# Optimization experiments

Hardware: AMD Instinct MI355X
Metric: run time of the kernel (lower is better)

Reference implementation:

```python
import jax, jax.numpy as jnp
import numpy as np

B, C, H, W = 2, 256, 64, 64
NUM_HEADS = 4
HEAD_DIM = C // NUM_HEADS
N = H * W


def setup_inputs() -> dict:
    key = jax.random.key(0)
    ks = jax.random.split(key, 10)
    x = jax.random.normal(ks[0], (B, C, H, W), dtype=jnp.float32)
    # mostly-True mask; diagonal forced True so every row has a valid key
    m = jax.random.uniform(ks[1], (B, N, N)) > 0.1
    spatial_mask = m | jnp.eye(N, dtype=bool)[None]
    s = 1.0 / np.sqrt(C)
    wq = jax.random.normal(ks[2], (C, C), dtype=jnp.float32) * s
    bq = jnp.zeros((C,), jnp.float32)
    wk = jax.random.normal(ks[3], (C, C), dtype=jnp.float32) * s
    bk = jnp.zeros((C,), jnp.float32)
    wv = jax.random.normal(ks[4], (C, C), dtype=jnp.float32) * s
    bv = jnp.zeros((C,), jnp.float32)
    # torch zero-inits out_proj; use random weights for a non-trivial baseline
    wo = jax.random.normal(ks[5], (C, C), dtype=jnp.float32) * s
    bo = jnp.zeros((C,), jnp.float32)
    return {"x": x, "spatial_mask": spatial_mask, "wq": wq, "bq": bq,
            "wk": wk, "bk": bk, "wv": wv, "bv": bv, "wo": wo, "bo": bo}


def reference(x, spatial_mask, wq, bq, wk, bk, wv, bv, wo, bo):
    b, c, h, w = x.shape
    n = h * w
    nh, hd = NUM_HEADS, HEAD_DIM
    scale = hd ** -0.5
    x_flat = x.reshape(b, c, n).transpose(0, 2, 1)           # [b, n, c]
    q = (x_flat @ wq.T + bq).reshape(b, n, nh, hd).transpose(0, 2, 1, 3)
    k = (x_flat @ wk.T + bk).reshape(b, n, nh, hd).transpose(0, 2, 1, 3)
    v = (x_flat @ wv.T + bv).reshape(b, n, nh, hd).transpose(0, 2, 1, 3)
    logits = jnp.einsum('bhqd,bhkd->bhqk', q, k) * scale      # [b, nh, n, n]
    logits = jnp.where(spatial_mask[:, None], logits, -jnp.inf)
    attn = jax.nn.softmax(logits, axis=-1)                    # dropout = identity (eval)
    out = jnp.einsum('bhqk,bhkd->bhqd', attn, v)              # [b, nh, n, hd]
    out = out.transpose(0, 2, 1, 3).reshape(b, n, c)
    out = out @ wo.T + bo
    return out.transpose(0, 2, 1).reshape(b, c, h, w)
```

## Files before the change

### kernel.cpp

```cpp
#include <hip/hip_runtime.h>
#include <math.h>

namespace {
constexpr int B_    = 2;
constexpr int C_    = 256;
constexpr int NHEAD = 4;
constexpr int HDIM  = 64;
constexpr int NTOK  = 4096;
constexpr float SCALE = 0.125f;
constexpr float LOG2E = 1.44269504f;
}

typedef _Float16 half8  __attribute__((ext_vector_type(8)));
typedef _Float16 half4  __attribute__((ext_vector_type(4)));
typedef __fp16   fp16x2 __attribute__((ext_vector_type(2)));
typedef float    floatx4 __attribute__((ext_vector_type(4)));
typedef int      int4v   __attribute__((ext_vector_type(4)));
typedef unsigned int uint2v __attribute__((ext_vector_type(2)));

__device__ __forceinline__ void plswap32(int &a, int &b) {
#if __has_builtin(__builtin_amdgcn_permlane32_swap)
    const uint2v r = __builtin_amdgcn_permlane32_swap((unsigned)a, (unsigned)b, false, false);
    a = (int)r[0]; b = (int)r[1];
#else
    asm volatile("s_nop 1\n\tv_permlane32_swap_b32 %0, %1\n\ts_nop 1"
                 : "+v"(a), "+v"(b));
#endif
}
__device__ __forceinline__ void plswap16(int &a, int &b) {
#if __has_builtin(__builtin_amdgcn_permlane16_swap)
    const uint2v r = __builtin_amdgcn_permlane16_swap((unsigned)a, (unsigned)b, false, false);
    a = (int)r[0]; b = (int)r[1];
#else
    asm volatile("s_nop 1\n\tv_permlane16_swap_b32 %0, %1\n\ts_nop 1"
                 : "+v"(a), "+v"(b));
#endif
}

__device__ __forceinline__ void gload_lds16(const _Float16* g, _Float16* l, int lane) {
#if __has_builtin(__builtin_amdgcn_global_load_lds)
    __builtin_amdgcn_global_load_lds(
        (const __attribute__((address_space(1))) void*)g,
        (__attribute__((address_space(3))) void*)l, 16, 0, 0);
#else
    *(half8*)((char*)l + lane * 16) = *(const half8*)g;
#endif
}

__global__ __launch_bounds__(256) void pack_mask(
    const unsigned int* __restrict__ m32, unsigned int* __restrict__ packed)
{
    int c0 = 0, c1 = 0, c2 = 0, c3 = 0;
    #pragma unroll
    for (int i = 0; i < 16; i++) {
        const unsigned int d = m32[i];
        c0 += (d == 0x00000001u);
        c1 += (d == 0x3F803F80u);
        c2 += (d == 0x3F800000u);
        c3 += (d == 0x01010101u);
    }
    int fmt = 1, best = c1;
    if (c0 > best) { best = c0; fmt = 0; }
    if (c2 > best) { best = c2; fmt = 2; }
    if (c3 > best) { best = c3; fmt = 3; }

    const unsigned int W = blockIdx.x * 256 + threadIdx.x;
    unsigned int bits = 0;
    if (fmt == 1) {
        const uint4* p4 = (const uint4*)(m32 + (size_t)W * 16);
        #pragma unroll
        for (int i = 0; i < 4; i++) {
            const uint4 v = p4[i];
            const unsigned int d[4] = { v.x, v.y, v.z, v.w };
            #pragma unroll
            for (int j = 0; j < 4; j++) {
                const int e = i * 8 + j * 2;
                bits |= ((d[j] & 0xFFFFu) ? 1u : 0u) << e;
                bits |= ((d[j] >> 16)     ? 1u : 0u) << (e + 1);
            }
        }
    } else if (fmt != 3) {
        const uint4* p4 = (const uint4*)(m32 + (size_t)W * 32);
        #pragma unroll
        for (int i = 0; i < 8; i++) {
            const uint4 v = p4[i];
            bits |= (v.x ? 1u : 0u) << (i * 4 + 0);
            bits |= (v.y ? 1u : 0u) << (i * 4 + 1);
            bits |= (v.z ? 1u : 0u) << (i * 4 + 2);
            bits |= (v.w ? 1u : 0u) << (i * 4 + 3);
        }
    } else {
        const uint4* p4 = (const uint4*)(m32 + (size_t)W * 8);
        #pragma unroll
        for (int i = 0; i < 2; i++) {
            const uint4 v = p4[i];
            const unsigned int d[4] = { v.x, v.y, v.z, v.w };
            #pragma unroll
            for (int j = 0; j < 4; j++) {
                const int e = (i * 4 + j) * 4;
                bits |= ((d[j] & 0x000000FFu) ? 1u : 0u) << (e + 0);
                bits |= ((d[j] & 0x0000FF00u) ? 1u : 0u) << (e + 1);
                bits |= ((d[j] & 0x00FF0000u) ? 1u : 0u) << (e + 2);
                bits |= ((d[j] & 0xFF000000u) ? 1u : 0u) << (e + 3);
            }
        }
    }
    packed[W] = bits;
}

__global__ __launch_bounds__(256) void qkv_mfma(
    const float* __restrict__ x,
    const float* __restrict__ wq, const float* __restrict__ bq,
    const float* __restrict__ wk, const float* __restrict__ bk,
    const float* __restrict__ wv, const float* __restrict__ bv,
    _Float16* __restrict__ qo, _Float16* __restrict__ ko,
    _Float16* __restrict__ vo)
{
    const int nt = blockIdx.x;
    const int b  = blockIdx.y;
    const int p  = blockIdx.z;

    const float* w; const float* bias;
    if (p == 0)      { w = wq; bias = bq; }
    else if (p == 1) { w = wk; bias = bk; }
    else             { w = wv; bias = bv; }

    const int t    = threadIdx.x;
    const int wid  = t >> 6;
    const int lane = t & 63;
    const int quad = lane >> 4;
    const int l15  = lane & 15;
    const int n0   = nt * 64;

    __shared__ _Float16 xsh[64 * 264];
    __shared__ _Float16 wsh[64 * 72];
    __shared__ _Float16 tbuf[64 * 72];

    const int srow = t >> 2;
    const int sc   = (t & 3) * 16;

    {
        const int cr = t >> 4;
        const int nu = (t & 15) * 4;
        const float* xb = x + (size_t)b * C_ * NTOK;
        #pragma unroll
        for (int cc = 0; cc < 16; cc++) {
            const int cl = cc * 16 + cr;
            const float4 v = *(const float4*)&xb[(size_t)cl * NTOK + n0 + nu];
            xsh[(nu + 0) * 264 + cl] = (_Float16)v.x;
            xsh[(nu + 1) * 264 + cl] = (_Float16)v.y;
            xsh[(nu + 2) * 264 + cl] = (_Float16)v.z;
            xsh[(nu + 3) * 264 + cl] = (_Float16)v.w;
        }
    }

    for (int h = 0; h < NHEAD; h++) {
        const int co0 = h * 64;
        floatx4 acc[4];
        #pragma unroll
        for (int i = 0; i < 4; i++) acc[i] = (floatx4)0.f;

        for (int c0 = 0; c0 < C_; c0 += 64) {
            {
                const float* wr = &w[(size_t)(co0 + srow) * C_ + c0 + sc];
                half8 h0, h1;
                #pragma unroll
                for (int u = 0; u < 2; u++) {
                    const float4 a = *(const float4*)&wr[u * 4];
                    h0[u*4+0]=(_Float16)a.x; h0[u*4+1]=(_Float16)a.y;
                    h0[u*4+2]=(_Float16)a.z; h0[u*4+3]=(_Float16)a.w;
                }
                #pragma unroll
                for (int u = 0; u < 2; u++) {
                    const float4 a = *(const float4*)&wr[8 + u * 4];
                    h1[u*4+0]=(_Float16)a.x; h1[u*4+1]=(_Float16)a.y;
                    h1[u*4+2]=(_Float16)a.z; h1[u*4+3]=(_Float16)a.w;
                }
                *(half8*)&wsh[srow * 72 + sc]     = h0;
                *(half8*)&wsh[srow * 72 + sc + 8] = h1;
            }
            __syncthreads();
            const half8 a0 = *(const half8*)&wsh[(wid * 16 + l15) * 72 + quad * 8];
            const half8 a1 = *(const half8*)&wsh[(wid * 16 + l15) * 72 + 32 + quad * 8];
            #pragma unroll
            for (int nt2 = 0; nt2 < 4; nt2++) {
                const half8 b0 = *(const half8*)&xsh[(nt2 * 16 + l15) * 264 + c0 + quad * 8];
                const half8 b1 = *(const half8*)&xsh[(nt2 * 16 + l15) * 264 + c0 + 32 + quad * 8];
                acc[nt2] = __builtin_amdgcn_mfma_f32_16x16x32_f16(a0, b0, acc[nt2], 0, 0, 0);
                acc[nt2] = __builtin_amdgcn_mfma_f32_16x16x32_f16(a1, b1, acc[nt2], 0, 0, 0);
            }
            __syncthreads();
        }

        const float4 bb4 = *(const float4*)&bias[co0 + wid * 16 + quad * 4];
        const float bb[4] = { bb4.x, bb4.y, bb4.z, bb4.w };

        if (p < 2) {
            const float osc = (p == 0) ? (SCALE * LOG2E) : 1.0f;
            #pragma unroll
            for (int nt2 = 0; nt2 < 4; nt2++) {
                half4 hv;
                #pragma unroll
                for (int i = 0; i < 4; i++)
                    hv[i] = (_Float16)((acc[nt2][i] + bb[i]) * osc);
                *(half4*)&tbuf[(nt2 * 16 + l15) * 72 + wid * 16 + quad * 4] = hv;
            }
            __syncthreads();
            _Float16* dh = (p == 0 ? qo : ko) + (size_t)(b * NHEAD + h) * NTOK * HDIM;
            const half8 o0 = *(const half8*)&tbuf[srow * 72 + sc];
            const half8 o1 = *(const half8*)&tbuf[srow * 72 + sc + 8];
            *(half8*)&dh[(size_t)(n0 + srow) * HDIM + sc]     = o0;
            *(half8*)&dh[(size_t)(n0 + srow) * HDIM + sc + 8] = o1;
        } else {
            #pragma unroll
            for (int nt2 = 0; nt2 < 4; nt2++)
                #pragma unroll
                for (int i = 0; i < 4; i++)
                    tbuf[(wid * 16 + quad * 4 + i) * 72 + nt2 * 16 + l15] =
                        (_Float16)(acc[nt2][i] + bb[i]);
            __syncthreads();
            _Float16* vth = vo + (size_t)(b * NHEAD + h) * HDIM * NTOK;
            const half8 o0 = *(const half8*)&tbuf[srow * 72 + sc];
            const half8 o1 = *(const half8*)&tbuf[srow * 72 + sc + 8];
            *(half8*)&vth[(size_t)srow * NTOK + n0 + sc]     = o0;
            *(half8*)&vth[(size_t)srow * NTOK + n0 + sc + 8] = o1;
        }
        __syncthreads();
    }
}

__global__ __launch_bounds__(512) void attn(
    const _Float16* __restrict__ q, const _Float16* __restrict__ k,
    const _Float16* __restrict__ vt, const unsigned int* __restrict__ mpacked,
    _Float16* __restrict__ ao)
{
    const int b  = blockIdx.z;
    const int h  = blockIdx.y;
    const int q0 = blockIdx.x * 64;
    const int t    = threadIdx.x;
    const int w    = t >> 6;
    const int lane = t & 63;
    const int quad = lane >> 4;
    const int l15  = lane & 15;
    const int half = w >> 2;
    const int w4   = w & 3;
    const int koff = half * (NTOK / 2);

    __shared__ __align__(16) char smem_raw[65536];
    _Float16* const sbase = (_Float16*)(smem_raw + half * 32768);

    const size_t head_off = (size_t)(b * NHEAD + h) * NTOK * HDIM;
    const _Float16* qb  = q  + head_off;
    const _Float16* kb  = k  + head_off;
    const _Float16* vtb = vt + head_off;
    const unsigned int* mrow = mpacked + (size_t)b * NTOK * 128;

    const int qrow = q0 + w4 * 16 + l15;
    half8 aq0 = *(const half8*)&qb[(size_t)qrow * HDIM + quad * 8];
    half8 aq1 = *(const half8*)&qb[(size_t)qrow * HDIM + 32 + quad * 8];
    const unsigned int* mq = &mrow[(size_t)qrow * 128];

    const int jr  = l15 & 7;
    const int xs0 = (quad ^ jr) << 3;
    const int xs1 = ((quad + 4) ^ jr) << 3;

    uint2 mw = *(const uint2*)&mq[koff >> 5];
    uint2 mw_nxt = mw;

    float l_loc = 0.f;
    floatx4 o_acc[4];
    #pragma unroll
    for (int i = 0; i < 4; i++) o_acc[i] = (floatx4)0.f;

#define STAGE(WO, K0N)                                                        \
    {                                                                         \
        const int rl = lane >> 3;                       \
        const int xc = ((lane & 7) ^ rl) << 3;        \
        const int c0 = w4 * 2, c1 = c0 + 1;                                   \
        gload_lds16(&kb[(size_t)((K0N) + c0 * 8 + rl) * HDIM + xc],           \
                    &sbase[(WO) + c0 * 512], lane);                           \
        gload_lds16(&kb[(size_t)((K0N) + c1 * 8 + rl) * HDIM + xc],           \
                    &sbase[(WO) + c1 * 512], lane);                           \
        gload_lds16(&vtb[(size_t)(c0 * 8 + rl) * NTOK + (K0N) + xc],          \
                    &sbase[(WO) + 4096 + c0 * 512], lane);                    \
        gload_lds16(&vtb[(size_t)(c1 * 8 + rl) * NTOK + (K0N) + xc],          \
                    &sbase[(WO) + 4096 + c1 * 512], lane);                    \
    }

    STAGE(0, koff)
    __syncthreads();

#define SOFTMAX_CT(CT, WORD, SH, Pa, Pb)                                          \
    {                                                                             \
        const unsigned nib = ((WORD) >> ((SH) + quad * 4)) & 0xFu;                \
        const float p0 = __builtin_amdgcn_exp2f((nib & 1u) ? sa[CT][0] : -3.0e38f);\
        const float p1 = __builtin_amdgcn_exp2f((nib & 2u) ? sa[CT][1] : -3.0e38f);\
        const float p2 = __builtin_amdgcn_exp2f((nib & 4u) ? sa[CT][2] : -3.0e38f);\
        const float p3 = __builtin_amdgcn_exp2f((nib & 8u) ? sa[CT][3] : -3.0e38f);\
        l_loc += (p0 + p1) + (p2 + p3);                                           \
        Pa = __builtin_bit_cast(int, __builtin_amdgcn_cvt_pkrtz(p0, p1));         \
        Pb = __builtin_bit_cast(int, __builtin_amdgcn_cvt_pkrtz(p2, p3));         \
    }

#define ATTN_TILE(RO, WO, KT, PF)                                                 \
    {                                                                             \
        if (PF) {                                                                 \
            const int k0n = koff + (KT) * 64 + 64;                                \
            STAGE(WO, k0n)                                                        \
            mw_nxt = *(const uint2*)&mq[k0n >> 5];                                \
        }                                                                         \
        floatx4 sa[4];                                                            \
        __builtin_amdgcn_s_setprio(1);                                            \
        _Pragma("unroll")                                                         \
        for (int ct = 0; ct < 4; ct++) {                                          \
            sa[ct] = (floatx4)0.f;                                                \
            const half8 ka0 = *(const half8*)&sbase[(RO) + (ct*16 + l15)*64 + xs0];\
            const half8 ka1 = *(const half8*)&sbase[(RO) + (ct*16 + l15)*64 + xs1];\
            sa[ct] = __builtin_amdgcn_mfma_f32_16x16x32_f16(ka0, aq0, sa[ct], 0, 0, 0);     \
            sa[ct] = __builtin_amdgcn_mfma_f32_16x16x32_f16(ka1, aq1, sa[ct], 0, 0, 0);     \
        }                                                                         \
        __builtin_amdgcn_s_setprio(0);                                            \
        int P00, P01, P10, P11, P20, P21, P30, P31;                               \
        SOFTMAX_CT(0, mw.x, 0,  P00, P01)                                         \
        SOFTMAX_CT(1, mw.x, 16, P10, P11)                                         \
        SOFTMAX_CT(2, mw.y, 0,  P20, P21)                                         \
        SOFTMAX_CT(3, mw.y, 16, P30, P31)                                         \
        mw = mw_nxt;                                                              \
                                                   \
        plswap32(P00, P10); plswap32(P01, P11);                                   \
        plswap32(P20, P30); plswap32(P21, P31);                                   \
                                               \
        plswap16(P00, P10); plswap16(P01, P11);                                   \
        plswap16(P20, P30); plswap16(P21, P31);                                   \
        const half8 pb0 = __builtin_bit_cast(half8, (int4v){P00, P01, P10, P11}); \
        const half8 pb1 = __builtin_bit_cast(half8, (int4v){P20, P21, P30, P31}); \
        __builtin_amdgcn_s_setprio(1);                                            \
        _Pragma("unroll")                                                         \
        for (int dt = 0; dt < 4; dt++) {                                          \
            const half8 va0 = *(const half8*)&sbase[(RO) + 4096 + (dt*16 + l15)*64 + xs0];\
            const half8 va1 = *(const half8*)&sbase[(RO) + 4096 + (dt*16 + l15)*64 + xs1];\
            o_acc[dt] = __builtin_amdgcn_mfma_f32_16x16x32_f16(va0, pb0, o_acc[dt], 0, 0, 0);      \
            o_acc[dt] = __builtin_amdgcn_mfma_f32_16x16x32_f16(va1, pb1, o_acc[dt], 0, 0, 0);      \
        }                                                                         \
        __builtin_amdgcn_s_setprio(0);                                            \
        __syncthreads();                                                          \
    }

    for (int kt2 = 0; kt2 < 15; kt2++) {
        ATTN_TILE(0,    8192, 2 * kt2,     1)
        ATTN_TILE(8192, 0,    2 * kt2 + 1, 1)
    }
    ATTN_TILE(0,    8192, 30, 1)
    ATTN_TILE(8192, 0,    31, 0)

#undef ATTN_TILE
#undef SOFTMAX_CT
#undef STAGE

    l_loc += __shfl_xor(l_loc, 16, 64);
    l_loc += __shfl_xor(l_loc, 32, 64);

    float* oex = (float*)smem_raw;
    float* lex = (float*)(smem_raw + 16384);
    if (w >= 4) {
        float* dst = &oex[((size_t)(w - 4) * 64 + lane) * 16];
        #pragma unroll
        for (int dt = 0; dt < 4; dt++)
            *(floatx4*)&dst[dt * 4] = o_acc[dt];
        if (quad == 0) lex[(w - 4) * 16 + l15] = l_loc;
    }
    __syncthreads();
    if (w < 4) {
        const float* src = &oex[((size_t)w * 64 + lane) * 16];
        const float lt = l_loc + lex[w * 16 + l15];
        const float inv = (lt > 0.f) ? (1.0f / lt) : 0.f;
        _Float16* aob = ao + ((size_t)b * NTOK + q0 + w * 16 + l15) * C_ + h * 64;
        #pragma unroll
        for (int dt = 0; dt < 4; dt++) {
            const floatx4 o2 = *(const floatx4*)&src[dt * 4];
            half4 r;
            #pragma unroll
            for (int rr = 0; rr < 4; rr++)
                r[rr] = (_Float16)((o_acc[dt][rr] + o2[rr]) * inv);
            *(half4*)&aob[dt * 16 + quad * 4] = r;
        }
    }
}

__global__ __launch_bounds__(256) void out_mfma(
    const _Float16* __restrict__ ao, const float* __restrict__ wo,
    const float* __restrict__ bo, float* __restrict__ out)
{
    const int nt  = blockIdx.x;
    const int cot = blockIdx.y;
    const int b   = blockIdx.z;
    const int t    = threadIdx.x;
    const int wid  = t >> 6;
    const int lane = t & 63;
    const int quad = lane >> 4;
    const int l15  = lane & 15;
    const int n0  = nt * 64;
    const int co0 = cot * 64;

    __shared__ _Float16 wsh[64 * 72];
    __shared__ _Float16 ash[64 * 72];
    __shared__ float    tf[64 * 68];

    const int srow = t >> 2;
    const int sc   = (t & 3) * 16;

    floatx4 acc[4];
    #pragma unroll
    for (int i = 0; i < 4; i++) acc[i] = (floatx4)0.f;

    const _Float16* aob = ao + ((size_t)b * NTOK + n0) * C_;

    for (int c0 = 0; c0 < C_; c0 += 64) {
        {
            const float* wr = &wo[(size_t)(co0 + srow) * C_ + c0 + sc];
            half8 h0, h1;
            #pragma unroll
            for (int u = 0; u < 2; u++) {
                const float4 a = *(const float4*)&wr[u * 4];
                h0[u*4+0]=(_Float16)a.x; h0[u*4+1]=(_Float16)a.y;
                h0[u*4+2]=(_Float16)a.z; h0[u*4+3]=(_Float16)a.w;
            }
            #pragma unroll
            for (int u = 0; u < 2; u++) {
                const float4 a = *(const float4*)&wr[8 + u * 4];
                h1[u*4+0]=(_Float16)a.x; h1[u*4+1]=(_Float16)a.y;
                h1[u*4+2]=(_Float16)a.z; h1[u*4+3]=(_Float16)a.w;
            }
            *(half8*)&wsh[srow * 72 + sc]     = h0;
            *(half8*)&wsh[srow * 72 + sc + 8] = h1;
        }
        {
            const _Float16* ar = &aob[(size_t)srow * C_ + c0 + sc];
            *(half8*)&ash[srow * 72 + sc]     = *(const half8*)&ar[0];
            *(half8*)&ash[srow * 72 + sc + 8] = *(const half8*)&ar[8];
        }
        __syncthreads();
        const half8 a0 = *(const half8*)&wsh[(wid * 16 + l15) * 72 + quad * 8];
        const half8 a1 = *(const half8*)&wsh[(wid * 16 + l15) * 72 + 32 + quad * 8];
        #pragma unroll
        for (int nt2 = 0; nt2 < 4; nt2++) {
            const half8 b0 = *(const half8*)&ash[(nt2 * 16 + l15) * 72 + quad * 8];
            const half8 b1 = *(const half8*)&ash[(nt2 * 16 + l15) * 72 + 32 + quad * 8];
            acc[nt2] = __builtin_amdgcn_mfma_f32_16x16x32_f16(a0, b0, acc[nt2], 0, 0, 0);
            acc[nt2] = __builtin_amdgcn_mfma_f32_16x16x32_f16(a1, b1, acc[nt2], 0, 0, 0);
        }
        __syncthreads();
    }

    #pragma unroll
    for (int nt2 = 0; nt2 < 4; nt2++)
        #pragma unroll
        for (int i = 0; i < 4; i++)
            tf[(wid * 16 + quad * 4 + i) * 68 + nt2 * 16 + l15] = acc[nt2][i];
    __syncthreads();

    const int row = t >> 2;
    const int c4  = (t & 3) * 16;
    const float bb = bo[co0 + row];
    float* orow = &out[((size_t)(b * C_ + co0 + row)) * NTOK + n0 + c4];
    #pragma unroll
    for (int u = 0; u < 4; u++) {
        float4 v = *(const float4*)&tf[row * 68 + c4 + u * 4];
        v.x += bb; v.y += bb; v.z += bb; v.w += bb;
        *(float4*)&orow[u * 4] = v;
    }
}

extern "C" void kernel_launch(void* const* d_in, const int* in_sizes, int n_in,
                              void* d_out, int out_size, void* d_ws, size_t ws_size,
                              hipStream_t stream) {
    const float* x    = (const float*)d_in[0];
    const void*  mask = d_in[1];
    const float* wq   = (const float*)d_in[2];
    const float* bq   = (const float*)d_in[3];
    const float* wk   = (const float*)d_in[4];
    const float* bk   = (const float*)d_in[5];
    const float* wv   = (const float*)d_in[6];
    const float* bv   = (const float*)d_in[7];
    const float* wo   = (const float*)d_in[8];
    const float* bo   = (const float*)d_in[9];
    float* out = (float*)d_out;

    const size_t qkv_elems = (size_t)B_ * NHEAD * NTOK * HDIM;
    _Float16* wsh = (_Float16*)d_ws;
    _Float16* qbuf  = wsh;
    _Float16* kbuf  = wsh + qkv_elems;
    _Float16* vtbuf = wsh + 2 * qkv_elems;
    _Float16* aobuf = wsh + 3 * qkv_elems;
    unsigned int* mpacked = (unsigned int*)(wsh + 4 * qkv_elems);

    pack_mask<<<dim3((B_ * NTOK * 128) / 256), 256, 0, stream>>>(
        (const unsigned int*)mask, mpacked);
    qkv_mfma<<<dim3(NTOK / 64, B_, 3), 256, 0, stream>>>(
        x, wq, bq, wk, bk, wv, bv, qbuf, kbuf, vtbuf);
    attn<<<dim3(NTOK / 64, NHEAD, B_), 512, 0, stream>>>(
        qbuf, kbuf, vtbuf, mpacked, aobuf);
    out_mfma<<<dim3(NTOK / 64, C_ / 64, B_), 256, 0, stream>>>(
        aobuf, wo, bo, out);
}
```

Baseline: 296.4 us.

## Pre-convert projection weights to fp16 once and read MFMA operands directly

Adds a small kernel that converts the four projection weight matrices to fp16 once per call, so the QKV and output projection kernels no longer convert fp32 weights per tile. Both projection kernels drop their LDS staging of weight tiles, and the output kernel also drops LDS staging of the attention output, loading MFMA operands straight from global memory with no per-iteration barriers. This removes redundant conversion work and synchronization, but adds a kernel launch and relies on cache for reuse of operands that LDS used to share across waves.

```diff
diff --git a/kernel.cpp b/kernel.cpp
--- a/kernel.cpp
+++ b/kernel.cpp
@@ -47,6 +47,23 @@
 #endif
 }
 
+__global__ __launch_bounds__(256) void wprep(
+    const float* __restrict__ wq, const float* __restrict__ wk,
+    const float* __restrict__ wv, const float* __restrict__ wo,
+    _Float16* __restrict__ w16)
+{
+    const float* src = (blockIdx.y == 0) ? wq :
+                       (blockIdx.y == 1) ? wk :
+                       (blockIdx.y == 2) ? wv : wo;
+    const int i8 = (blockIdx.x * 256 + threadIdx.x) * 8;
+    const float4 a = *(const float4*)&src[i8];
+    const float4 b = *(const float4*)&src[i8 + 4];
+    half8 h;
+    h[0]=(_Float16)a.x; h[1]=(_Float16)a.y; h[2]=(_Float16)a.z; h[3]=(_Float16)a.w;
+    h[4]=(_Float16)b.x; h[5]=(_Float16)b.y; h[6]=(_Float16)b.z; h[7]=(_Float16)b.w;
+    *(half8*)&w16[(size_t)blockIdx.y * 65536 + i8] = h;
+}
+
 __global__ __launch_bounds__(256) void pack_mask(
     const unsigned int* __restrict__ m32, unsigned int* __restrict__ packed)
 {
@@ -109,10 +126,9 @@
 }
 
 __global__ __launch_bounds__(256) void qkv_mfma(
-    const float* __restrict__ x,
-    const float* __restrict__ wq, const float* __restrict__ bq,
-    const float* __restrict__ wk, const float* __restrict__ bk,
-    const float* __restrict__ wv, const float* __restrict__ bv,
+    const float* __restrict__ x, const _Float16* __restrict__ w16,
+    const float* __restrict__ bq, const float* __restrict__ bk,
+    const float* __restrict__ bv,
     _Float16* __restrict__ qo, _Float16* __restrict__ ko,
     _Float16* __restrict__ vo)
 {
@@ -120,10 +136,8 @@
     const int b  = blockIdx.y;
     const int p  = blockIdx.z;
 
-    const float* w; const float* bias;
-    if (p == 0)      { w = wq; bias = bq; }
-    else if (p == 1) { w = wk; bias = bk; }
-    else             { w = wv; bias = bv; }
+    const _Float16* w = w16 + (size_t)p * C_ * C_;
+    const float* bias = (p == 0) ? bq : (p == 1) ? bk : bv;
 
     const int t    = threadIdx.x;
     const int wid  = t >> 6;
@@ -133,7 +147,6 @@
     const int n0   = nt * 64;
 
     __shared__ _Float16 xsh[64 * 264];
-    __shared__ _Float16 wsh[64 * 72];
     __shared__ _Float16 tbuf[64 * 72];
 
     const int srow = t >> 2;
@@ -153,6 +166,9 @@
             xsh[(nu + 3) * 264 + cl] = (_Float16)v.w;
         }
     }
+    __syncthreads();
+
+    const _Float16* wrow = &w[(size_t)(wid * 16 + l15) * C_];
 
     for (int h = 0; h < NHEAD; h++) {
         const int co0 = h * 64;
@@ -160,28 +176,10 @@
         #pragma unroll
         for (int i = 0; i < 4; i++) acc[i] = (floatx4)0.f;
 
+        #pragma unroll
         for (int c0 = 0; c0 < C_; c0 += 64) {
-            {
-                const float* wr = &w[(size_t)(co0 + srow) * C_ + c0 + sc];
-                half8 h0, h1;
-                #pragma unroll
-                for (int u = 0; u < 2; u++) {
-                    const float4 a = *(const float4*)&wr[u * 4];
-                    h0[u*4+0]=(_Float16)a.x; h0[u*4+1]=(_Float16)a.y;
-                    h0[u*4+2]=(_Float16)a.z; h0[u*4+3]=(_Float16)a.w;
-                }
-                #pragma unroll
-                for (int u = 0; u < 2; u++) {
-                    const float4 a = *(const float4*)&wr[8 + u * 4];
-                    h1[u*4+0]=(_Float16)a.x; h1[u*4+1]=(_Float16)a.y;
-                    h1[u*4+2]=(_Float16)a.z; h1[u*4+3]=(_Float16)a.w;
-                }
-                *(half8*)&wsh[srow * 72 + sc]     = h0;
-                *(half8*)&wsh[srow * 72 + sc + 8] = h1;
-            }
-            __syncthreads();
-            const half8 a0 = *(const half8*)&wsh[(wid * 16 + l15) * 72 + quad * 8];
-            const half8 a1 = *(const half8*)&wsh[(wid * 16 + l15) * 72 + 32 + quad * 8];
+            const half8 a0 = *(const half8*)&wrow[(size_t)co0 * C_ + c0 + quad * 8];
+            const half8 a1 = *(const half8*)&wrow[(size_t)co0 * C_ + c0 + 32 + quad * 8];
             #pragma unroll
             for (int nt2 = 0; nt2 < 4; nt2++) {
                 const half8 b0 = *(const half8*)&xsh[(nt2 * 16 + l15) * 264 + c0 + quad * 8];
@@ -189,7 +187,6 @@
                 acc[nt2] = __builtin_amdgcn_mfma_f32_16x16x32_f16(a0, b0, acc[nt2], 0, 0, 0);
                 acc[nt2] = __builtin_amdgcn_mfma_f32_16x16x32_f16(a1, b1, acc[nt2], 0, 0, 0);
             }
-            __syncthreads();
         }
 
         const float4 bb4 = *(const float4*)&bias[co0 + wid * 16 + quad * 4];
@@ -326,10 +323,8 @@
         SOFTMAX_CT(2, mw.y, 0,  P20, P21)                                         \
         SOFTMAX_CT(3, mw.y, 16, P30, P31)                                         \
         mw = mw_nxt;                                                              \
-                                                   \
         plswap32(P00, P10); plswap32(P01, P11);                                   \
         plswap32(P20, P30); plswap32(P21, P31);                                   \
-                                               \
         plswap16(P00, P10); plswap16(P01, P11);                                   \
         plswap16(P20, P30); plswap16(P21, P31);                                   \
         const half8 pb0 = __builtin_bit_cast(half8, (int4v){P00, P01, P10, P11}); \
@@ -388,7 +383,7 @@
 }
 
 __global__ __launch_bounds__(256) void out_mfma(
-    const _Float16* __restrict__ ao, const float* __restrict__ wo,
+    const _Float16* __restrict__ ao, const _Float16* __restrict__ wo16,
     const float* __restrict__ bo, float* __restrict__ out)
 {
     const int nt  = blockIdx.x;
@@ -402,54 +397,26 @@
     const int n0  = nt * 64;
     const int co0 = cot * 64;
 
-    __shared__ _Float16 wsh[64 * 72];
-    __shared__ _Float16 ash[64 * 72];
-    __shared__ float    tf[64 * 68];
-
-    const int srow = t >> 2;
-    const int sc   = (t & 3) * 16;
+    __shared__ float tf[64 * 68];
 
     floatx4 acc[4];
     #pragma unroll
     for (int i = 0; i < 4; i++) acc[i] = (floatx4)0.f;
 
-    const _Float16* aob = ao + ((size_t)b * NTOK + n0) * C_;
-
+    const _Float16* wrow = &wo16[(size_t)(co0 + wid * 16 + l15) * C_];
+    const _Float16* aob  = ao + ((size_t)b * NTOK + n0) * C_;
+
+    #pragma unroll
     for (int c0 = 0; c0 < C_; c0 += 64) {
-        {
-            const float* wr = &wo[(size_t)(co0 + srow) * C_ + c0 + sc];
-            half8 h0, h1;
-            #pragma unroll
-            for (int u = 0; u < 2; u++) {
-                const float4 a = *(const float4*)&wr[u * 4];
-                h0[u*4+0]=(_Float16)a.x; h0[u*4+1]=(_Float16)a.y;
-                h0[u*4+2]=(_Float16)a.z; h0[u*4+3]=(_Float16)a.w;
-            }
-            #pragma unroll
-            for (int u = 0; u < 2; u++) {
-                const float4 a = *(const float4*)&wr[8 + u * 4];
-                h1[u*4+0]=(_Float16)a.x; h1[u*4+1]=(_Float16)a.y;
-                h1[u*4+2]=(_Float16)a.z; h1[u*4+3]=(_Float16)a.w;
-            }
-            *(half8*)&wsh[srow * 72 + sc]     = h0;
-            *(half8*)&wsh[srow * 72 + sc + 8] = h1;
-        }
-        {
-            const _Float16* ar = &aob[(size_t)srow * C_ + c0 + sc];
-            *(half8*)&ash[srow * 72 + sc]     = *(const half8*)&ar[0];
-            *(half8*)&ash[srow * 72 + sc + 8] = *(const half8*)&ar[8];
-        }
-        __syncthreads();
-        const half8 a0 = *(const half8*)&wsh[(wid * 16 + l15) * 72 + quad * 8];
-        const half8 a1 = *(const half8*)&wsh[(wid * 16 + l15) * 72 + 32 + quad * 8];
+        const half8 a0 = *(const half8*)&wrow[c0 + quad * 8];
+        const half8 a1 = *(const half8*)&wrow[c0 + 32 + quad * 8];
         #pragma unroll
         for (int nt2 = 0; nt2 < 4; nt2++) {
-            const half8 b0 = *(const half8*)&ash[(nt2 * 16 + l15) * 72 + quad * 8];
-            const half8 b1 = *(const half8*)&ash[(nt2 * 16 + l15) * 72 + 32 + quad * 8];
+            const half8 b0 = *(const half8*)&aob[(size_t)(nt2 * 16 + l15) * C_ + c0 + quad * 8];
+            const half8 b1 = *(const half8*)&aob[(size_t)(nt2 * 16 + l15) * C_ + c0 + 32 + quad * 8];
             acc[nt2] = __builtin_amdgcn_mfma_f32_16x16x32_f16(a0, b0, acc[nt2], 0, 0, 0);
             acc[nt2] = __builtin_amdgcn_mfma_f32_16x16x32_f16(a1, b1, acc[nt2], 0, 0, 0);
         }
-        __syncthreads();
     }
 
     #pragma unroll
@@ -493,13 +460,15 @@
     _Float16* vtbuf = wsh + 2 * qkv_elems;
     _Float16* aobuf = wsh + 3 * qkv_elems;
     unsigned int* mpacked = (unsigned int*)(wsh + 4 * qkv_elems);
-
+    _Float16* w16buf = wsh + 4 * qkv_elems + 2 * (size_t)(B_ * NTOK * 128);
+
+    wprep<<<dim3(32, 4), 256, 0, stream>>>(wq, wk, wv, wo, w16buf);
     pack_mask<<<dim3((B_ * NTOK * 128) / 256), 256, 0, stream>>>(
         (const unsigned int*)mask, mpacked);
     qkv_mfma<<<dim3(NTOK / 64, B_, 3), 256, 0, stream>>>(
-        x, wq, bq, wk, bk, wv, bv, qbuf, kbuf, vtbuf);
+        x, w16buf, bq, bk, bv, qbuf, kbuf, vtbuf);
     attn<<<dim3(NTOK / 64, NHEAD, B_), 512, 0, stream>>>(
         qbuf, kbuf, vtbuf, mpacked, aobuf);
     out_mfma<<<dim3(NTOK / 64, C_ / 64, B_), 256, 0, stream>>>(
-        aobuf, wo, bo, out);
-}
+        aobuf, w16buf + 3 * 65536, bo, out);
+}
```

After: 293.8 us. About the same (-0.9%).
